# Performance work log

Measured on AMD Instinct MI355X. Metric: run time of the kernel, lower is better.

## Reference

```python
import jax, jax.numpy as jnp
import numpy as np

N = 50000   # num_nodes
E = 640000  # num_edges (avg degree ~12.8)
D = 128     # input_dim
H = 128     # hidden_dim
T = 100     # targets per head


def setup_inputs() -> dict:
    key = jax.random.key(0)
    ks = jax.random.split(key, 20)
    w = lambda k, s: jax.random.normal(k, s, jnp.float32) * 0.02
    return {
        "x": jax.random.normal(ks[0], (N, D), jnp.float32),
        "edge_index": jax.random.randint(ks[1], (2, E), 0, N, dtype=jnp.int32),
        "edge_weight": jax.random.uniform(ks[2], (E,), jnp.float32),
        "ace_idx": jax.random.randint(ks[3], (T,), 0, N, dtype=jnp.int32),
        "h2_idx": jax.random.randint(ks[4], (T,), 0, N, dtype=jnp.int32),
        "W1": w(ks[5], (D, H)), "b1": jnp.zeros((H,), jnp.float32),
        "W2": w(ks[6], (H, H)), "b2": jnp.zeros((H,), jnp.float32),
        "W3": w(ks[7], (H, H)), "b3": jnp.zeros((H,), jnp.float32),
        "Wh": w(ks[8], (H, H)), "bh": jnp.zeros((H,), jnp.float32),
        "Wace": w(ks[9], (H, 1)), "bace": jnp.zeros((1,), jnp.float32),
        "Wh2": w(ks[10], (H, 1)), "bh2": jnp.zeros((1,), jnp.float32),
    }


def gcn_conv(x, src, dst, ew, W, b):
    # PyG GCNConv: add self-loops (weight 1), symmetric D^-1/2 (A+I) D^-1/2, then XW + b
    n = x.shape[0]
    xw = x @ W                                             # [N, H]
    deg = jax.ops.segment_sum(ew, dst, num_segments=n) + 1.0  # +1 from self-loop
    dinv = jax.lax.rsqrt(jnp.maximum(deg, 1e-12))          # deg >= 1 here
    norm = dinv[src] * ew * dinv[dst]                      # per-edge coefficient
    agg = jax.ops.segment_sum(norm[:, None] * xw[src], dst, num_segments=n)
    agg = agg + (dinv * dinv)[:, None] * xw                # self-loop contribution
    return agg + b


def reference(x, edge_index, edge_weight, ace_idx, h2_idx,
              W1, b1, W2, b2, W3, b3, Wh, bh, Wace, bace, Wh2, bh2):
    src, dst = edge_index[0], edge_index[1]
    h = jax.nn.relu(gcn_conv(x, src, dst, edge_weight, W1, b1))
    h = jax.nn.relu(gcn_conv(h, src, dst, edge_weight, W2, b2))
    h = jax.nn.relu(gcn_conv(h, src, dst, edge_weight, W3, b3))
    # dropout is identity in eval mode
    h = jax.nn.relu(h @ Wh + bh)
    ace_pred = h[ace_idx] @ Wace + bace   # [T, 1]
    h2_pred = h[h2_idx] @ Wh2 + bh2       # [T, 1]
    return jnp.concatenate([ace_pred, h2_pred], axis=0)  # [2T, 1]
```

## Files before the change

### kernel.cpp

```cpp
#include <hip/hip_runtime.h>
#include <math.h>

constexpr int N = 50000;
constexpr int E = 640000;
constexpr int D = 128;
constexpr int T = 100;
constexpr int NB = (N + 255) / 256;
constexpr int NSH = 8;
constexpr float SC = 256.0f;
constexpr float SCINV = 1.0f / 256.0f;

typedef __attribute__((ext_vector_type(8))) _Float16 half8v;
typedef __attribute__((ext_vector_type(8))) unsigned short ushort8v;
typedef __attribute__((ext_vector_type(4))) float f32x4;


__global__ void deg_count_kernel(const float* __restrict__ ew, const int* __restrict__ dst,
                                 unsigned long long* __restrict__ degcnt) {
  int e = blockIdx.x * 256 + threadIdx.x;
  int shard = blockIdx.x & (NSH - 1);
  if (e < E) {
    unsigned int fx = (unsigned int)__float2uint_rn(ew[e] * 16777216.0f);
    atomicAdd(&degcnt[(size_t)shard * N + dst[e]],
              ((unsigned long long)fx << 32) | 1ull);
  }
}


__global__ __launch_bounds__(256) void scan_reduce_kernel(const uint2* __restrict__ degcnt,
                                                          int* __restrict__ bsum,
                                                          float* __restrict__ dinv) {
  __shared__ int part[256];
  int t = threadIdx.x;
  int i = blockIdx.x * 256 + t;
  int c = 0;
  if (i < N) {
    unsigned int cnt = 0, dg = 0;
#pragma unroll
    for (int s = 0; s < NSH; ++s) {
      uint2 p = degcnt[(size_t)s * N + i];
      cnt += p.x; dg += p.y;
    }
    c = (int)cnt;
    float d = (float)dg * (1.0f / 16777216.0f) + 1.0f;
    dinv[i] = 1.0f / sqrtf(d);
  }
  part[t] = c;
  __syncthreads();
#pragma unroll
  for (int off = 128; off; off >>= 1) {
    if (t < off) part[t] += part[t + off];
    __syncthreads();
  }
  if (t == 0) bsum[blockIdx.x] = part[0];
}


__global__ __launch_bounds__(256) void scan_apply_kernel(const uint2* __restrict__ degcnt,
                                                         const int* __restrict__ bsum,
                                                         int* __restrict__ offs,
                                                         int* __restrict__ cursor) {
  __shared__ int sb[256];
  __shared__ int part[256];
  int t = threadIdx.x;
  int i = blockIdx.x * 256 + t;
  sb[t] = (t < NB) ? bsum[t] : 0;
  int cs[NSH];
  int c = 0;
  if (i < N) {
#pragma unroll
    for (int s = 0; s < NSH; ++s) {
      cs[s] = (int)degcnt[(size_t)s * N + i].x;
      c += cs[s];
    }
  }
  part[t] = c;
  __syncthreads();
#pragma unroll
  for (int off = 1; off < 256; off <<= 1) {
    int u1 = (t >= off) ? sb[t - off] : 0;
    int u2 = (t >= off) ? part[t - off] : 0;
    __syncthreads();
    sb[t] += u1;
    part[t] += u2;
    __syncthreads();
  }
  int base = (blockIdx.x == 0) ? 0 : sb[blockIdx.x - 1];
  if (i < N) {
    int o = base + part[t] - c;
    offs[i] = o;
    int run = o;
#pragma unroll
    for (int s = 0; s < NSH; ++s) {
      cursor[(size_t)s * N + i] = run;
      run += cs[s];
    }
  }
  if (i == 0) offs[N] = E;
}


__global__ void fill_kernel(const int* __restrict__ src, const int* __restrict__ dst,
                            const float* __restrict__ ew, const float* __restrict__ dinv,
                            int* __restrict__ cursor, unsigned int* __restrict__ csr) {
  int e = blockIdx.x * 256 + threadIdx.x;
  int shard = blockIdx.x & (NSH - 1);
  if (e < E) {
    int s = src[e], d = dst[e];
    float c = dinv[s] * ew[e] * dinv[d];
    unsigned int fx = __float2uint_rn(c * 65536.0f);
    if (fx > 65535u) fx = 65535u;
    int pos = atomicAdd(&cursor[(size_t)shard * N + d], 1);
    csr[pos] = (fx << 16) | (unsigned int)s;
  }
}


__global__ void wprep_kernel(const float* __restrict__ W0, const float* __restrict__ W1,
                             const float* __restrict__ W2, unsigned short* __restrict__ wt,
                             unsigned short* __restrict__ w3kn) {
  int idx = blockIdx.x * 256 + threadIdx.x;
  int layer = idx >> 14;
  int r = idx & 16383;
  int k = r & 127, n = r >> 7;
  const float* W = layer == 0 ? W0 : layer == 1 ? W1 : W2;
  float v = W[k * D + n] * (layer == 0 ? SC : 1.0f);
  _Float16 h = (_Float16)v;
  unsigned short bits = *(unsigned short*)&h;
  wt[layer * 16384 + n * D + k] = bits;
  if (layer == 2) w3kn[k * D + n] = bits;
}


__global__ void mark_kernel(const int* __restrict__ ace_idx, const int* __restrict__ h2_idx,
                            const int* __restrict__ offs, const unsigned int* __restrict__ csr,
                            int* __restrict__ flags) {
  int t = blockIdx.x;
  int tid = threadIdx.x;
  int g = (t < T) ? ace_idx[t] : h2_idx[t - T];
  if (tid == 0) flags[g] = 1;
  int e0 = offs[g], e1 = offs[g + 1];
  for (int e = e0 + tid; e < e1; e += 64) flags[csr[e] & 0xffffu] = 1;
}


__global__ __launch_bounds__(256) void wl_reduce_kernel(const int* __restrict__ flags,
                                                        int* __restrict__ wsum) {
  __shared__ int part[256];
  int t = threadIdx.x;
  int i = blockIdx.x * 256 + t;
  part[t] = (i < N) ? flags[i] : 0;
  __syncthreads();
#pragma unroll
  for (int off = 128; off; off >>= 1) {
    if (t < off) part[t] += part[t + off];
    __syncthreads();
  }
  if (t == 0) wsum[blockIdx.x] = part[0];
}

__global__ __launch_bounds__(256) void wl_apply_kernel(const int* __restrict__ flags,
                                                       const int* __restrict__ wsum,
                                                       int* __restrict__ worklist,
                                                       int* __restrict__ wlcount) {
  __shared__ int sb[256];
  __shared__ int part[256];
  int t = threadIdx.x;
  int i = blockIdx.x * 256 + t;
  sb[t] = (t < NB) ? wsum[t] : 0;
  int f = (i < N) ? flags[i] : 0;
  part[t] = f;
  __syncthreads();
#pragma unroll
  for (int off = 1; off < 256; off <<= 1) {
    int u1 = (t >= off) ? sb[t - off] : 0;
    int u2 = (t >= off) ? part[t - off] : 0;
    __syncthreads();
    sb[t] += u1;
    part[t] += u2;
    __syncthreads();
  }
  int base = (blockIdx.x == 0) ? 0 : sb[blockIdx.x - 1];
  if (i < N && f) worklist[base + part[t] - f] = i;
  if (blockIdx.x == 0 && t == 0) wlcount[0] = sb[NB - 1];
}


__device__ inline void stage_B(const unsigned short* __restrict__ Wt,
                               unsigned short* __restrict__ Bl, int tid) {
  constexpr int SB = 136;
#pragma unroll
  for (int it = 0; it < 8; ++it) {
    int idx = tid + it * 256;
    int r = idx >> 4;
    int c8 = idx & 15;
    ushort8v v = *(const ushort8v*)&Wt[r * D + c8 * 8];
    *(ushort8v*)&Bl[r * SB + c8 * 8] = v;
  }
}

__device__ inline void mfma_core_and_store(
    const unsigned short* __restrict__ Bl, half8v (*a)[2],
    int row0, int rbase, int q, int n16, unsigned short* __restrict__ out) {
  constexpr int SB = 136;
  f32x4 acc[2][8] = {};
#pragma unroll
  for (int kc = 0; kc < 4; ++kc) {
    const int ko = kc * 32 + q * 8;
#pragma unroll
    for (int ct = 0; ct < 8; ++ct) {
      int n = ct * 16 + n16;
      half8v b = *(const half8v*)&Bl[n * SB + ko];
#pragma unroll
      for (int rt = 0; rt < 2; ++rt) {
        acc[rt][ct] = __builtin_amdgcn_mfma_f32_16x16x32_f16(a[kc][rt], b, acc[rt][ct], 0, 0, 0);
      }
    }
  }
#pragma unroll
  for (int rt = 0; rt < 2; ++rt) {
#pragma unroll
    for (int r = 0; r < 4; ++r) {
      int gr = row0 + rbase + rt * 16 + q * 4 + r;
      if (gr < N) {
#pragma unroll
        for (int ct = 0; ct < 8; ++ct) {
          int col = ct * 16 + n16;
          _Float16 h = (_Float16)acc[rt][ct][r];
          out[(size_t)gr * D + col] = *(unsigned short*)&h;
        }
      }
    }
  }
}

__global__ __launch_bounds__(256) void gemm_mfma_kernel(
    const unsigned short* __restrict__ A, const unsigned short* __restrict__ Wt,
    unsigned short* __restrict__ out) {
  constexpr int SB = 136;
  __shared__ unsigned short Bl[128 * SB];
  const int tid = threadIdx.x;
  const int row0 = blockIdx.x * 128;
  stage_B(Wt, Bl, tid);
  __syncthreads();

  const int w = tid >> 6, lane = tid & 63;
  const int q = lane >> 4, n16 = lane & 15;
  const int rbase = w * 32;
  size_t arow[2];
#pragma unroll
  for (int rt = 0; rt < 2; ++rt) {
    int gr = row0 + rbase + rt * 16 + n16;
    if (gr >= N) gr = N - 1;
    arow[rt] = (size_t)gr * D;
  }
  half8v a[4][2];
#pragma unroll
  for (int kc = 0; kc < 4; ++kc) {
    const int ko = kc * 32 + q * 8;
#pragma unroll
    for (int rt = 0; rt < 2; ++rt)
      a[kc][rt] = *(const half8v*)&A[arow[rt] + ko];
  }
  mfma_core_and_store(Bl, a, row0, rbase, q, n16, out);
}

__global__ __launch_bounds__(256) void gemm_mfma_f32_kernel(
    const float* __restrict__ A, const unsigned short* __restrict__ Wt,
    unsigned short* __restrict__ out) {
  constexpr int SB = 136;
  __shared__ unsigned short Bl[128 * SB];
  const int tid = threadIdx.x;
  const int row0 = blockIdx.x * 128;
  stage_B(Wt, Bl, tid);
  __syncthreads();

  const int w = tid >> 6, lane = tid & 63;
  const int q = lane >> 4, n16 = lane & 15;
  const int rbase = w * 32;
  size_t arow[2];
#pragma unroll
  for (int rt = 0; rt < 2; ++rt) {
    int gr = row0 + rbase + rt * 16 + n16;
    if (gr >= N) gr = N - 1;
    arow[rt] = (size_t)gr * D;
  }
  half8v a[4][2];
#pragma unroll
  for (int kc = 0; kc < 4; ++kc) {
    const int ko = kc * 32 + q * 8;
#pragma unroll
    for (int rt = 0; rt < 2; ++rt) {
      float4 v0 = *(const float4*)&A[arow[rt] + ko];
      float4 v1 = *(const float4*)&A[arow[rt] + ko + 4];
      half8v h;
      h[0] = (_Float16)v0.x; h[1] = (_Float16)v0.y;
      h[2] = (_Float16)v0.z; h[3] = (_Float16)v0.w;
      h[4] = (_Float16)v1.x; h[5] = (_Float16)v1.y;
      h[6] = (_Float16)v1.z; h[7] = (_Float16)v1.w;
      a[kc][rt] = h;
    }
  }
  mfma_core_and_store(Bl, a, row0, rbase, q, n16, out);
}


__global__ __launch_bounds__(256) void agg_kernel(
    const unsigned short* __restrict__ xwb, const unsigned int* __restrict__ csr,
    const int* __restrict__ offs, const float* __restrict__ dinv,
    const float* __restrict__ bias, unsigned short* __restrict__ oP) {
  int g = (blockIdx.x * 256 + threadIdx.x) >> 4;
  int lane = threadIdx.x & 15;

  float dv = dinv[g];
  float s = dv * dv;
  half8v xv = *(const half8v*)&xwb[(size_t)g * D + lane * 8];
  float acc[8];
#pragma unroll
  for (int i = 0; i < 8; ++i)
    acc[i] = fmaf(s, (float)xv[i], bias[lane * 8 + i] * SC);

  int e = offs[g], e1 = offs[g + 1];
  for (; e + 2 <= e1; e += 2) {
    unsigned int p0 = csr[e], p1 = csr[e + 1];
    float c0 = (float)(p0 >> 16) * (1.0f / 65536.0f);
    float c1 = (float)(p1 >> 16) * (1.0f / 65536.0f);
    half8v v0 = *(const half8v*)&xwb[(size_t)(p0 & 0xffffu) * D + lane * 8];
    half8v v1 = *(const half8v*)&xwb[(size_t)(p1 & 0xffffu) * D + lane * 8];
#pragma unroll
    for (int i = 0; i < 8; ++i) {
      acc[i] = fmaf(c0, (float)v0[i], acc[i]);
      acc[i] = fmaf(c1, (float)v1[i], acc[i]);
    }
  }
  if (e < e1) {
    unsigned int p = csr[e];
    float c = (float)(p >> 16) * (1.0f / 65536.0f);
    half8v v = *(const half8v*)&xwb[(size_t)(p & 0xffffu) * D + lane * 8];
#pragma unroll
    for (int i = 0; i < 8; ++i) acc[i] = fmaf(c, (float)v[i], acc[i]);
  }

  half8v hv;
#pragma unroll
  for (int i = 0; i < 8; ++i)
    hv[i] = (_Float16)fmaxf(acc[i], 0.f);
  *(half8v*)&oP[(size_t)g * D + lane * 8] = hv;
}


__global__ __launch_bounds__(256) void agg_wl_kernel(
    const unsigned short* __restrict__ xwb, const unsigned int* __restrict__ csr,
    const int* __restrict__ offs, const float* __restrict__ dinv,
    const float* __restrict__ bias, const int* __restrict__ worklist,
    const int* __restrict__ wlcount, unsigned short* __restrict__ oP) {
  int idx = (blockIdx.x * 256 + threadIdx.x) >> 4;
  if (idx >= wlcount[0]) return;
  int g = worklist[idx];
  int lane = threadIdx.x & 15;

  float dv = dinv[g];
  float s = dv * dv;
  half8v xv = *(const half8v*)&xwb[(size_t)g * D + lane * 8];
  float acc[8];
#pragma unroll
  for (int i = 0; i < 8; ++i)
    acc[i] = fmaf(s, (float)xv[i], bias[lane * 8 + i] * SC);

  int e = offs[g], e1 = offs[g + 1];
  for (; e + 2 <= e1; e += 2) {
    unsigned int p0 = csr[e], p1 = csr[e + 1];
    float c0 = (float)(p0 >> 16) * (1.0f / 65536.0f);
    float c1 = (float)(p1 >> 16) * (1.0f / 65536.0f);
    half8v v0 = *(const half8v*)&xwb[(size_t)(p0 & 0xffffu) * D + lane * 8];
    half8v v1 = *(const half8v*)&xwb[(size_t)(p1 & 0xffffu) * D + lane * 8];
#pragma unroll
    for (int i = 0; i < 8; ++i) {
      acc[i] = fmaf(c0, (float)v0[i], acc[i]);
      acc[i] = fmaf(c1, (float)v1[i], acc[i]);
    }
  }
  if (e < e1) {
    unsigned int p = csr[e];
    float c = (float)(p >> 16) * (1.0f / 65536.0f);
    half8v v = *(const half8v*)&xwb[(size_t)(p & 0xffffu) * D + lane * 8];
#pragma unroll
    for (int i = 0; i < 8; ++i) acc[i] = fmaf(c, (float)v[i], acc[i]);
  }

  half8v hv;
#pragma unroll
  for (int i = 0; i < 8; ++i)
    hv[i] = (_Float16)fmaxf(acc[i], 0.f);
  *(half8v*)&oP[(size_t)g * D + lane * 8] = hv;
}


__global__ __launch_bounds__(256) void layer3_heads_kernel(
    const unsigned short* __restrict__ P0, const unsigned int* __restrict__ csr,
    const int* __restrict__ offs, const float* __restrict__ dinv,
    const float* __restrict__ b3, const unsigned short* __restrict__ w3kn,
    const float* __restrict__ Wh, const float* __restrict__ bh,
    const int* __restrict__ ace_idx, const int* __restrict__ h2_idx,
    const float* __restrict__ Wace, const float* __restrict__ bace,
    const float* __restrict__ Wh2, const float* __restrict__ bh2,
    float* __restrict__ out) {
  __shared__ float sacc[16][128];
  __shared__ unsigned short w3l[16384];
  __shared__ float svec[128];
  __shared__ float h3v[128];
  __shared__ float psum[2];
  int t = blockIdx.x;
  int tid = threadIdx.x;
  int node; const float* whead; float bhead;
  if (t < T) { node = ace_idx[t];     whead = Wace; bhead = bace[0]; }
  else       { node = h2_idx[t - T];  whead = Wh2;  bhead = bh2[0]; }

#pragma unroll
  for (int it = 0; it < 8; ++it) {
    int idx = tid + it * 256;
    *(ushort8v*)&w3l[idx * 8] = *(const ushort8v*)&w3kn[idx * 8];
  }

  int grp = tid >> 4, lane = tid & 15;
  float a[8] = {};
  if (grp == 0) {
    float dv = dinv[node];
    float s = dv * dv;
    half8v xv = *(const half8v*)&P0[(size_t)node * D + lane * 8];
#pragma unroll
    for (int i = 0; i < 8; ++i) a[i] = s * (float)xv[i];
  }
  int e0 = offs[node], e1 = offs[node + 1];
  for (int e = e0 + grp; e < e1; e += 16) {
    unsigned int p = csr[e];
    float c = (float)(p >> 16) * (1.0f / 65536.0f);
    half8v v = *(const half8v*)&P0[(size_t)(p & 0xffffu) * D + lane * 8];
#pragma unroll
    for (int i = 0; i < 8; ++i) a[i] = fmaf(c, (float)v[i], a[i]);
  }
#pragma unroll
  for (int i = 0; i < 8; ++i) sacc[grp][lane * 8 + i] = a[i];
  __syncthreads();

  if (tid < 128) {
    float s = 0.f;
#pragma unroll
    for (int gp = 0; gp < 16; ++gp) s += sacc[gp][tid];
    svec[tid] = s;
  }
  __syncthreads();

  if (tid < 128) {
    float y = b3[tid] * SC;
#pragma unroll 16
    for (int k = 0; k < 128; ++k) {
      _Float16 wv = *(const _Float16*)&w3l[k * D + tid];
      y = fmaf(svec[k], (float)wv, y);
    }
    h3v[tid] = fmaxf(y, 0.f) * SCINV;
  }
  __syncthreads();

  float v = 0.f;
  if (tid < 128) {
    float acc = bh[tid];
#pragma unroll 16
    for (int k = 0; k < 128; ++k)
      acc = fmaf(h3v[k], Wh[k * D + tid], acc);
    v = fmaxf(acc, 0.f) * whead[tid];
  }
#pragma unroll
  for (int off = 32; off; off >>= 1) v += __shfl_down(v, off, 64);
  if (tid < 128 && (tid & 63) == 0) psum[tid >> 6] = v;
  __syncthreads();
  if (tid == 0) out[t] = psum[0] + psum[1] + bhead;
}


extern "C" void kernel_launch(void* const* d_in, const int* in_sizes, int n_in,
                              void* d_out, int out_size, void* d_ws, size_t ws_size,
                              hipStream_t stream) {
  const float* x    = (const float*)d_in[0];
  const int*   ei   = (const int*)d_in[1];
  const float* ew   = (const float*)d_in[2];
  const int*   ace  = (const int*)d_in[3];
  const int*   h2   = (const int*)d_in[4];
  const float* W1 = (const float*)d_in[5];  const float* b1 = (const float*)d_in[6];
  const float* W2 = (const float*)d_in[7];  const float* b2 = (const float*)d_in[8];
  const float* W3 = (const float*)d_in[9];  const float* b3 = (const float*)d_in[10];
  const float* Wh = (const float*)d_in[11]; const float* bh = (const float*)d_in[12];
  const float* Wace = (const float*)d_in[13]; const float* bace = (const float*)d_in[14];
  const float* Wh2  = (const float*)d_in[15]; const float* bh2  = (const float*)d_in[16];
  const int* src = ei;
  const int* dst = ei + E;

  char* w = (char*)d_ws;
  unsigned long long* degcnt = (unsigned long long*)w;  w += (size_t)NSH * N * 8;
  int*   flags  = (int*)w;                w += N * 4;
  float* dinv   = (float*)w;              w += N * 4;
  int*   offs   = (int*)w;                w += (N + 4) * 4;
  int*   cursor = (int*)w;                w += (size_t)NSH * N * 4;
  int*   bsum   = (int*)w;                w += 256 * 4;
  int*   wsum   = (int*)w;                w += 256 * 4;
  int*   wlcount= (int*)w;                w += 16 * 4;
  int*   worklist=(int*)w;                w += N * 4;
  unsigned short* wt = (unsigned short*)w; w += 3 * 16384 * 2;
  unsigned short* w3kn = (unsigned short*)w; w += 16384 * 2;
  unsigned int* csr = (unsigned int*)w;   w += (size_t)E * 4;
  unsigned short* xwb = (unsigned short*)w; w += (size_t)N * D * 2;
  unsigned short* P0  = (unsigned short*)w; w += (size_t)N * D * 2;
  unsigned short* P1  = (unsigned short*)w; w += (size_t)N * D * 2;

  hipMemsetAsync(degcnt, 0, (size_t)NSH * N * 8 + (size_t)N * 4, stream);
  deg_count_kernel<<<(E + 255) / 256, 256, 0, stream>>>(ew, dst, degcnt);
  scan_reduce_kernel<<<NB, 256, 0, stream>>>((const uint2*)degcnt, bsum, dinv);
  scan_apply_kernel<<<NB, 256, 0, stream>>>((const uint2*)degcnt, bsum, offs, cursor);
  fill_kernel<<<(E + 255) / 256, 256, 0, stream>>>(src, dst, ew, dinv, cursor, csr);
  wprep_kernel<<<192, 256, 0, stream>>>(W1, W2, W3, wt, w3kn);
  mark_kernel<<<2 * T, 64, 0, stream>>>(ace, h2, offs, csr, flags);
  wl_reduce_kernel<<<NB, 256, 0, stream>>>(flags, wsum);
  wl_apply_kernel<<<NB, 256, 0, stream>>>(flags, wsum, worklist, wlcount);

  const int GB = (N + 127) / 128;
  const int AG = N * 16 / 256;

  gemm_mfma_f32_kernel<<<GB, 256, 0, stream>>>(x, wt + 0 * 16384, xwb);
  agg_kernel<<<AG, 256, 0, stream>>>(xwb, csr, offs, dinv, b1, P1);
  gemm_mfma_kernel<<<GB, 256, 0, stream>>>(P1, wt + 1 * 16384, xwb);
  agg_wl_kernel<<<AG, 256, 0, stream>>>(xwb, csr, offs, dinv, b2, worklist, wlcount, P0);
  layer3_heads_kernel<<<2 * T, 256, 0, stream>>>(P0, csr, offs, dinv, b3, w3kn,
                                                 Wh, bh, ace, h2, Wace, bace, Wh2, bh2,
                                                 (float*)d_out);
}
```

Measured before the change: 255.7 us.

## Fuse graph preprocessing kernels into one cooperative kernel with grid syncs

Replaces the memset plus eight small preprocessing launches (degree count, scans, CSR fill, weight prep, target marking, worklist build) with one persistent cooperative kernel of 1024 blocks that separates phases with grid.sync(). The neighbor marking for target nodes moves into the CSR fill pass through a per-node target flag, so the separate mark kernel and its second read of the CSR are no longer needed. This is meant to cut launch gaps and tail idle time between the tiny kernels. In exchange it pays for six grid-wide barriers and runs the edge loops grid-stride on a fixed grid.

```diff
diff --git a/kernel.cpp b/kernel.cpp
--- a/kernel.cpp
+++ b/kernel.cpp
@@ -1,5 +1,8 @@
 #include <hip/hip_runtime.h>
+#include <hip/hip_cooperative_groups.h>
 #include <math.h>
+
+namespace cg = cooperative_groups;
 
 constexpr int N = 50000;
 constexpr int E = 640000;
@@ -7,6 +10,8 @@
 constexpr int T = 100;
 constexpr int NB = (N + 255) / 256;
 constexpr int NSH = 8;
+constexpr int GBLK = 1024;
+constexpr int GTHR = GBLK * 256;
 constexpr float SC = 256.0f;
 constexpr float SCINV = 1.0f / 256.0f;
 
@@ -15,174 +20,164 @@
 typedef __attribute__((ext_vector_type(4))) float f32x4;
 
 
-__global__ void deg_count_kernel(const float* __restrict__ ew, const int* __restrict__ dst,
-                                 unsigned long long* __restrict__ degcnt) {
-  int e = blockIdx.x * 256 + threadIdx.x;
-  int shard = blockIdx.x & (NSH - 1);
-  if (e < E) {
-    unsigned int fx = (unsigned int)__float2uint_rn(ew[e] * 16777216.0f);
-    atomicAdd(&degcnt[(size_t)shard * N + dst[e]],
-              ((unsigned long long)fx << 32) | 1ull);
-  }
-}
-
-
-__global__ __launch_bounds__(256) void scan_reduce_kernel(const uint2* __restrict__ degcnt,
-                                                          int* __restrict__ bsum,
-                                                          float* __restrict__ dinv) {
-  __shared__ int part[256];
-  int t = threadIdx.x;
-  int i = blockIdx.x * 256 + t;
-  int c = 0;
-  if (i < N) {
-    unsigned int cnt = 0, dg = 0;
-#pragma unroll
-    for (int s = 0; s < NSH; ++s) {
-      uint2 p = degcnt[(size_t)s * N + i];
-      cnt += p.x; dg += p.y;
-    }
-    c = (int)cnt;
-    float d = (float)dg * (1.0f / 16777216.0f) + 1.0f;
-    dinv[i] = 1.0f / sqrtf(d);
-  }
-  part[t] = c;
-  __syncthreads();
-#pragma unroll
-  for (int off = 128; off; off >>= 1) {
-    if (t < off) part[t] += part[t + off];
-    __syncthreads();
-  }
-  if (t == 0) bsum[blockIdx.x] = part[0];
-}
-
-
-__global__ __launch_bounds__(256) void scan_apply_kernel(const uint2* __restrict__ degcnt,
-                                                         const int* __restrict__ bsum,
-                                                         int* __restrict__ offs,
-                                                         int* __restrict__ cursor) {
+__global__ __launch_bounds__(256, 4) void build_kernel(
+    const float* __restrict__ ew, const int* __restrict__ src, const int* __restrict__ dst,
+    const int* __restrict__ ace_idx, const int* __restrict__ h2_idx,
+    const float* __restrict__ W0, const float* __restrict__ W1, const float* __restrict__ W2,
+    unsigned long long* __restrict__ degcnt, float* __restrict__ dinv,
+    int* __restrict__ offs, int* __restrict__ cursor,
+    int* __restrict__ bsum, int* __restrict__ wsum,
+    int* __restrict__ wlcount, int* __restrict__ worklist,
+    unsigned short* __restrict__ wt, unsigned short* __restrict__ w3kn,
+    unsigned int* __restrict__ csr, int* __restrict__ flags, int* __restrict__ tflag) {
+  cg::grid_group grid = cg::this_grid();
+  const int tid = threadIdx.x;
+  const int gtid = blockIdx.x * 256 + tid;
   __shared__ int sb[256];
   __shared__ int part[256];
-  int t = threadIdx.x;
-  int i = blockIdx.x * 256 + t;
-  sb[t] = (t < NB) ? bsum[t] : 0;
-  int cs[NSH];
-  int c = 0;
-  if (i < N) {
-#pragma unroll
-    for (int s = 0; s < NSH; ++s) {
-      cs[s] = (int)degcnt[(size_t)s * N + i].x;
-      c += cs[s];
-    }
-  }
-  part[t] = c;
-  __syncthreads();
-#pragma unroll
-  for (int off = 1; off < 256; off <<= 1) {
-    int u1 = (t >= off) ? sb[t - off] : 0;
-    int u2 = (t >= off) ? part[t - off] : 0;
+
+  for (int i = gtid; i < NSH * N; i += GTHR) degcnt[i] = 0ull;
+  for (int i = gtid; i < N; i += GTHR) { flags[i] = 0; tflag[i] = 0; }
+  for (int idx = gtid; idx < 3 * 16384; idx += GTHR) {
+    int layer = idx >> 14;
+    int r = idx & 16383;
+    int k = r & 127, n = r >> 7;
+    const float* W = layer == 0 ? W0 : layer == 1 ? W1 : W2;
+    float v = W[k * D + n] * (layer == 0 ? SC : 1.0f);
+    _Float16 h = (_Float16)v;
+    unsigned short bits = *(unsigned short*)&h;
+    wt[layer * 16384 + n * D + k] = bits;
+    if (layer == 2) w3kn[k * D + n] = bits;
+  }
+  grid.sync();
+
+  {
+    int shard = blockIdx.x & (NSH - 1);
+    for (int e = gtid; e < E; e += GTHR) {
+      unsigned int fx = __float2uint_rn(ew[e] * 16777216.0f);
+      atomicAdd(&degcnt[(size_t)shard * N + dst[e]],
+                ((unsigned long long)fx << 32) | 1ull);
+    }
+    if (gtid < 2 * T) {
+      int g = (gtid < T) ? ace_idx[gtid] : h2_idx[gtid - T];
+      tflag[g] = 1;
+    }
+  }
+  grid.sync();
+
+  if (blockIdx.x < NB) {
+    int i = blockIdx.x * 256 + tid;
+    int c = 0;
+    if (i < N) {
+      unsigned int cnt = 0, dg = 0;
+#pragma unroll
+      for (int s = 0; s < NSH; ++s) {
+        uint2 p = ((const uint2*)degcnt)[(size_t)s * N + i];
+        cnt += p.x; dg += p.y;
+      }
+      c = (int)cnt;
+      float d = (float)dg * (1.0f / 16777216.0f) + 1.0f;
+      dinv[i] = 1.0f / sqrtf(d);
+    }
+    part[tid] = c;
     __syncthreads();
-    sb[t] += u1;
-    part[t] += u2;
+#pragma unroll
+    for (int off = 128; off; off >>= 1) {
+      if (tid < off) part[tid] += part[tid + off];
+      __syncthreads();
+    }
+    if (tid == 0) bsum[blockIdx.x] = part[0];
+  }
+  grid.sync();
+
+  if (blockIdx.x < NB) {
+    int i = blockIdx.x * 256 + tid;
+    sb[tid] = (tid < NB) ? bsum[tid] : 0;
+    int cs[NSH];
+    int c = 0;
+    if (i < N) {
+#pragma unroll
+      for (int s = 0; s < NSH; ++s) {
+        cs[s] = (int)((const uint2*)degcnt)[(size_t)s * N + i].x;
+        c += cs[s];
+      }
+    }
+    part[tid] = c;
     __syncthreads();
-  }
-  int base = (blockIdx.x == 0) ? 0 : sb[blockIdx.x - 1];
-  if (i < N) {
-    int o = base + part[t] - c;
-    offs[i] = o;
-    int run = o;
-#pragma unroll
-    for (int s = 0; s < NSH; ++s) {
-      cursor[(size_t)s * N + i] = run;
-      run += cs[s];
-    }
-  }
-  if (i == 0) offs[N] = E;
-}
-
-
-__global__ void fill_kernel(const int* __restrict__ src, const int* __restrict__ dst,
-                            const float* __restrict__ ew, const float* __restrict__ dinv,
-                            int* __restrict__ cursor, unsigned int* __restrict__ csr) {
-  int e = blockIdx.x * 256 + threadIdx.x;
-  int shard = blockIdx.x & (NSH - 1);
-  if (e < E) {
-    int s = src[e], d = dst[e];
-    float c = dinv[s] * ew[e] * dinv[d];
-    unsigned int fx = __float2uint_rn(c * 65536.0f);
-    if (fx > 65535u) fx = 65535u;
-    int pos = atomicAdd(&cursor[(size_t)shard * N + d], 1);
-    csr[pos] = (fx << 16) | (unsigned int)s;
-  }
-}
-
-
-__global__ void wprep_kernel(const float* __restrict__ W0, const float* __restrict__ W1,
-                             const float* __restrict__ W2, unsigned short* __restrict__ wt,
-                             unsigned short* __restrict__ w3kn) {
-  int idx = blockIdx.x * 256 + threadIdx.x;
-  int layer = idx >> 14;
-  int r = idx & 16383;
-  int k = r & 127, n = r >> 7;
-  const float* W = layer == 0 ? W0 : layer == 1 ? W1 : W2;
-  float v = W[k * D + n] * (layer == 0 ? SC : 1.0f);
-  _Float16 h = (_Float16)v;
-  unsigned short bits = *(unsigned short*)&h;
-  wt[layer * 16384 + n * D + k] = bits;
-  if (layer == 2) w3kn[k * D + n] = bits;
-}
-
-
-__global__ void mark_kernel(const int* __restrict__ ace_idx, const int* __restrict__ h2_idx,
-                            const int* __restrict__ offs, const unsigned int* __restrict__ csr,
-                            int* __restrict__ flags) {
-  int t = blockIdx.x;
-  int tid = threadIdx.x;
-  int g = (t < T) ? ace_idx[t] : h2_idx[t - T];
-  if (tid == 0) flags[g] = 1;
-  int e0 = offs[g], e1 = offs[g + 1];
-  for (int e = e0 + tid; e < e1; e += 64) flags[csr[e] & 0xffffu] = 1;
-}
-
-
-__global__ __launch_bounds__(256) void wl_reduce_kernel(const int* __restrict__ flags,
-                                                        int* __restrict__ wsum) {
-  __shared__ int part[256];
-  int t = threadIdx.x;
-  int i = blockIdx.x * 256 + t;
-  part[t] = (i < N) ? flags[i] : 0;
-  __syncthreads();
-#pragma unroll
-  for (int off = 128; off; off >>= 1) {
-    if (t < off) part[t] += part[t + off];
+#pragma unroll
+    for (int off = 1; off < 256; off <<= 1) {
+      int u1 = (tid >= off) ? sb[tid - off] : 0;
+      int u2 = (tid >= off) ? part[tid - off] : 0;
+      __syncthreads();
+      sb[tid] += u1;
+      part[tid] += u2;
+      __syncthreads();
+    }
+    int base = (blockIdx.x == 0) ? 0 : sb[blockIdx.x - 1];
+    if (i < N) {
+      int o = base + part[tid] - c;
+      offs[i] = o;
+      int run = o;
+#pragma unroll
+      for (int s = 0; s < NSH; ++s) {
+        cursor[(size_t)s * N + i] = run;
+        run += cs[s];
+      }
+    }
+    if (i == 0) offs[N] = E;
+  }
+  grid.sync();
+
+  {
+    int shard = blockIdx.x & (NSH - 1);
+    for (int e = gtid; e < E; e += GTHR) {
+      int s = src[e], d = dst[e];
+      float c = dinv[s] * ew[e] * dinv[d];
+      unsigned int fx = __float2uint_rn(c * 65536.0f);
+      if (fx > 65535u) fx = 65535u;
+      int pos = atomicAdd(&cursor[(size_t)shard * N + d], 1);
+      csr[pos] = (fx << 16) | (unsigned int)s;
+      if (tflag[d]) flags[s] = 1;
+    }
+    if (gtid < 2 * T) {
+      int g = (gtid < T) ? ace_idx[gtid] : h2_idx[gtid - T];
+      flags[g] = 1;
+    }
+  }
+  grid.sync();
+
+  if (blockIdx.x < NB) {
+    int i = blockIdx.x * 256 + tid;
+    part[tid] = (i < N) ? flags[i] : 0;
     __syncthreads();
-  }
-  if (t == 0) wsum[blockIdx.x] = part[0];
-}
-
-__global__ __launch_bounds__(256) void wl_apply_kernel(const int* __restrict__ flags,
-                                                       const int* __restrict__ wsum,
-                                                       int* __restrict__ worklist,
-                                                       int* __restrict__ wlcount) {
-  __shared__ int sb[256];
-  __shared__ int part[256];
-  int t = threadIdx.x;
-  int i = blockIdx.x * 256 + t;
-  sb[t] = (t < NB) ? wsum[t] : 0;
-  int f = (i < N) ? flags[i] : 0;
-  part[t] = f;
-  __syncthreads();
-#pragma unroll
-  for (int off = 1; off < 256; off <<= 1) {
-    int u1 = (t >= off) ? sb[t - off] : 0;
-    int u2 = (t >= off) ? part[t - off] : 0;
+#pragma unroll
+    for (int off = 128; off; off >>= 1) {
+      if (tid < off) part[tid] += part[tid + off];
+      __syncthreads();
+    }
+    if (tid == 0) wsum[blockIdx.x] = part[0];
+  }
+  grid.sync();
+
+  if (blockIdx.x < NB) {
+    int i = blockIdx.x * 256 + tid;
+    sb[tid] = (tid < NB) ? wsum[tid] : 0;
+    int f = (i < N) ? flags[i] : 0;
+    part[tid] = f;
     __syncthreads();
-    sb[t] += u1;
-    part[t] += u2;
-    __syncthreads();
-  }
-  int base = (blockIdx.x == 0) ? 0 : sb[blockIdx.x - 1];
-  if (i < N && f) worklist[base + part[t] - f] = i;
-  if (blockIdx.x == 0 && t == 0) wlcount[0] = sb[NB - 1];
+#pragma unroll
+    for (int off = 1; off < 256; off <<= 1) {
+      int u1 = (tid >= off) ? sb[tid - off] : 0;
+      int u2 = (tid >= off) ? part[tid - off] : 0;
+      __syncthreads();
+      sb[tid] += u1;
+      part[tid] += u2;
+      __syncthreads();
+    }
+    int base = (blockIdx.x == 0) ? 0 : sb[blockIdx.x - 1];
+    if (i < N && f) worklist[base + part[tid] - f] = i;
+    if (blockIdx.x == 0 && tid == 0) wlcount[0] = sb[NB - 1];
+  }
 }
 
 
@@ -498,6 +493,7 @@
   char* w = (char*)d_ws;
   unsigned long long* degcnt = (unsigned long long*)w;  w += (size_t)NSH * N * 8;
   int*   flags  = (int*)w;                w += N * 4;
+  int*   tflag  = (int*)w;                w += N * 4;
   float* dinv   = (float*)w;              w += N * 4;
   int*   offs   = (int*)w;                w += (N + 4) * 4;
   int*   cursor = (int*)w;                w += (size_t)NSH * N * 4;
@@ -512,15 +508,16 @@
   unsigned short* P0  = (unsigned short*)w; w += (size_t)N * D * 2;
   unsigned short* P1  = (unsigned short*)w; w += (size_t)N * D * 2;
 
-  hipMemsetAsync(degcnt, 0, (size_t)NSH * N * 8 + (size_t)N * 4, stream);
-  deg_count_kernel<<<(E + 255) / 256, 256, 0, stream>>>(ew, dst, degcnt);
-  scan_reduce_kernel<<<NB, 256, 0, stream>>>((const uint2*)degcnt, bsum, dinv);
-  scan_apply_kernel<<<NB, 256, 0, stream>>>((const uint2*)degcnt, bsum, offs, cursor);
-  fill_kernel<<<(E + 255) / 256, 256, 0, stream>>>(src, dst, ew, dinv, cursor, csr);
-  wprep_kernel<<<192, 256, 0, stream>>>(W1, W2, W3, wt, w3kn);
-  mark_kernel<<<2 * T, 64, 0, stream>>>(ace, h2, offs, csr, flags);
-  wl_reduce_kernel<<<NB, 256, 0, stream>>>(flags, wsum);
-  wl_apply_kernel<<<NB, 256, 0, stream>>>(flags, wsum, worklist, wlcount);
+  {
+    void* args[] = {
+      (void*)&ew, (void*)&src, (void*)&dst, (void*)&ace, (void*)&h2,
+      (void*)&W1, (void*)&W2, (void*)&W3,
+      (void*)&degcnt, (void*)&dinv, (void*)&offs, (void*)&cursor,
+      (void*)&bsum, (void*)&wsum, (void*)&wlcount, (void*)&worklist,
+      (void*)&wt, (void*)&w3kn, (void*)&csr, (void*)&flags, (void*)&tflag};
+    hipLaunchCooperativeKernel((void*)build_kernel, dim3(GBLK), dim3(256),
+                               args, 0, stream);
+  }
 
   const int GB = (N + 127) / 128;
   const int AG = N * 16 / 256;
```

Result: slower. 899.2 us (+251.6%).
